# Kernel tuning notes

Measured on AMD Instinct MI355X. Metric: run time of the kernel, lower is better.

## Reference

```python
import jax, jax.numpy as jnp
import numpy as np

SP, WD, H, HID = 8, 3, 8, 256
D = HID // H
TEMP = 0.1


def setup_inputs() -> dict:
    key = jax.random.key(0)
    ks = jax.random.split(key, 14)
    B, Lq, Lk, F = 4, 1024, 2048, SP + WD
    s = 0.05
    return {
        "q_fp": jax.random.normal(ks[0], (B, Lq, F), jnp.float32),
        "v_ret": jax.random.normal(ks[1], (B, Lk, F), jnp.float32),
        "pi_star": jax.random.uniform(ks[2], (B, Lq, Lk), jnp.float32),
        "Wq_s": jax.random.normal(ks[3], (HID, SP), jnp.float32) * s,
        "bq_s": jax.random.normal(ks[4], (HID,), jnp.float32) * s,
        "Wk_s": jax.random.normal(ks[5], (HID, SP), jnp.float32) * s,
        "bk_s": jax.random.normal(ks[6], (HID,), jnp.float32) * s,
        "Wq_w": jax.random.normal(ks[7], (HID, WD), jnp.float32) * s,
        "bq_w": jax.random.normal(ks[8], (HID,), jnp.float32) * s,
        "Wk_w": jax.random.normal(ks[9], (HID, WD), jnp.float32) * s,
        "bk_w": jax.random.normal(ks[10], (HID,), jnp.float32) * s,
        "Wv": jax.random.normal(ks[11], (HID, F), jnp.float32) * s,
        "bv": jnp.zeros((HID,), jnp.float32),
        "Wo": jax.random.normal(ks[12], (HID, HID), jnp.float32) * s,
        "bo": jnp.zeros((HID,), jnp.float32),
        "wave_blend": jnp.array(0.5, jnp.float32),
    }


def _proj(x, W, b):
    # x: [B, L, F_in] -> [B, H, L, D]
    B, L, _ = x.shape
    return (x @ W.T + b).reshape(B, L, H, D).transpose(0, 2, 1, 3)


def reference(q_fp, v_ret, pi_star, Wq_s, bq_s, Wk_s, bk_s, Wq_w, bq_w, Wk_w, bk_w, Wv, bv, Wo, bo, wave_blend):
    B, Lq, _ = q_fp.shape
    # split streams: first SP dims spatial, next WD dims wave (F == SP+WD)
    q_sp, q_wv = q_fp[..., :SP], q_fp[..., SP:SP + WD]
    k_sp, k_wv = v_ret[..., :SP], v_ret[..., SP:SP + WD]
    # structural branch: scaled dot product
    q_struct = _proj(q_sp, Wq_s, bq_s)
    k_struct = _proj(k_sp, Wk_s, bk_s)
    spatial_logits = jnp.einsum('bhqd,bhkd->bhqk', q_struct, k_struct) / np.float32(np.sqrt(D))
    # wave branch: negative squared euclidean distance via norm expansion
    q_wp = _proj(q_wv, Wq_w, bq_w)
    k_wp = _proj(k_wv, Wk_w, bk_w)
    qn = jnp.sum(q_wp * q_wp, axis=-1)[..., :, None]   # [B,H,Lq,1]
    kn = jnp.sum(k_wp * k_wp, axis=-1)[..., None, :]   # [B,H,1,Lk]
    qk = jnp.einsum('bhqd,bhkd->bhqk', q_wp, k_wp)
    wave_logits = -(qn + kn - 2.0 * qk) / np.float32(TEMP)
    alpha = jax.nn.sigmoid(wave_blend)
    transport_mask = jnp.log(jnp.clip(pi_star, 1e-9, None))[:, None]  # [B,1,Lq,Lk]
    attn = jax.nn.softmax((1.0 - alpha) * spatial_logits + alpha * wave_logits + transport_mask, axis=-1)
    values = _proj(v_ret, Wv, bv)  # [B,H,Lk,D]
    ctx = jnp.einsum('bhqk,bhkd->bhqd', attn, values)
    ctx = ctx.transpose(0, 2, 1, 3).reshape(B, Lq, HID)
    return ctx @ Wo.T + bo
```

## Files before the change

### kernel.cpp

```cpp
#include <hip/hip_runtime.h>
#include <hip/hip_bf16.h>
#include <cstdint>

#define B_    4
#define LQ    1024
#define LK    2048
#define FEAT  11
#define SP_   8
#define WD_   3
#define H_    8
#define HID_  256
#define LOG2E 1.4426950408889634f
#define SPLIT 2
#define KPS   (LK / SPLIT)
#define ITERS (KPS / 64)

typedef __attribute__((ext_vector_type(4))) float f32x4;
typedef __attribute__((ext_vector_type(8))) short bf16x8;
typedef __attribute__((ext_vector_type(4))) short s16x4;

__device__ __forceinline__ float sigmoidf_(float x) { return 1.f / (1.f + __expf(-x)); }

__device__ __forceinline__ short f2bf(float f) {
  unsigned u = __float_as_uint(f);
  u += 0x7fffu + ((u >> 16) & 1u);
  return (short)(u >> 16);
}
__device__ __forceinline__ float bf2f(short s) {
  return __uint_as_float(((unsigned)(unsigned short)s) << 16);
}

__device__ __forceinline__ void gl_lds16(const void* g, void* l) {
  __builtin_amdgcn_global_load_lds(
      (const __attribute__((address_space(1))) unsigned int*)g,
      (__attribute__((address_space(3))) unsigned int*)l, 16, 0, 0);
}

__global__ __launch_bounds__(256) void proj_q_kernel(
    const float* __restrict__ q_fp, const float* __restrict__ Wq_s,
    const float* __restrict__ bq_s, const float* __restrict__ Wq_w,
    const float* __restrict__ bq_w, const float* __restrict__ wb,
    short* __restrict__ Qh)
{
  const int row = blockIdx.x;
  const int t   = threadIdx.x;
  const float alpha = sigmoidf_(wb[0]);
  const float c1 = (1.f - alpha) * 0.17677669529663687f * LOG2E;
  const float c2 = 2.f * alpha * 10.f * LOG2E;

  const float* x = q_fp + (size_t)row * FEAT;
  float xs[FEAT];
  #pragma unroll
  for (int f = 0; f < FEAT; ++f) xs[f] = x[f];

  float s = bq_s[t];
  #pragma unroll
  for (int f = 0; f < SP_; ++f) s += xs[f] * Wq_s[t * SP_ + f];
  float w = bq_w[t];
  #pragma unroll
  for (int f = 0; f < WD_; ++f) w += xs[SP_ + f] * Wq_w[t * WD_ + f];

  const int h = t >> 5, d = t & 31;
  const int b = row >> 10, q = row & (LQ - 1);
  const size_t base = ((size_t)(b * H_ + h) * LQ + q) * 64;
  Qh[base + d]      = f2bf(c1 * s);
  Qh[base + 32 + d] = f2bf(c2 * w);
}

__global__ __launch_bounds__(256) void projk_pack_kernel(
    const float* __restrict__ v_ret, const float* __restrict__ Wk_s,
    const float* __restrict__ bk_s, const float* __restrict__ Wk_w,
    const float* __restrict__ bk_w, const float* __restrict__ Wv,
    const float* __restrict__ bv,   const float* __restrict__ wb,
    short* __restrict__ KV, float* __restrict__ kb)
{
  __shared__ float ldsv[64][33];
  const int blk = blockIdx.x, bh = blockIdx.y;
  const int b = bh >> 3, h = bh & 7;
  const int t = threadIdx.x;
  const int kl = t >> 2, part = t & 3;
  const int k = blk * 64 + kl;
  const float alpha = sigmoidf_(wb[0]);

  const float* x = v_ret + (size_t)(b * LK + k) * FEAT;
  float xs[FEAT];
  #pragma unroll
  for (int f = 0; f < FEAT; ++f) xs[f] = x[f];

  float s8[8], w8[8], v8[8];
  #pragma unroll
  for (int i = 0; i < 8; ++i) {
    const int d = h * 32 + part * 8 + i;
    float s = bk_s[d];
    #pragma unroll
    for (int f = 0; f < SP_; ++f) s += xs[f] * Wk_s[d * SP_ + f];
    float w = bk_w[d];
    #pragma unroll
    for (int f = 0; f < WD_; ++f) w += xs[SP_ + f] * Wk_w[d * WD_ + f];
    float v = bv[d];
    #pragma unroll
    for (int f = 0; f < FEAT; ++f) v += xs[f] * Wv[d * FEAT + f];
    s8[i] = s; w8[i] = w; v8[i] = v;
    ldsv[kl][part * 8 + i] = v;
  }

  float sq = 0.f;
  #pragma unroll
  for (int i = 0; i < 8; ++i) sq += w8[i] * w8[i];
  sq += __shfl_xor(sq, 1);
  sq += __shfl_xor(sq, 2);
  if (part == 0) kb[(size_t)bh * LK + k] = -10.f * alpha * LOG2E * sq;

  const int a  = kl >> 5;
  const int bb = (kl >> 2) & 1;
  const int p  = kl - a * 32 - bb * 4;
  const int lo = ((p >> 3) << 2) | (p & 3);
  const int t4 = a * 2 + bb;
  const size_t base = ((size_t)bh * 32 + blk) * 768;

  bf16x8 hs, hw;
  #pragma unroll
  for (int i = 0; i < 8; ++i) { hs[i] = f2bf(s8[i]); hw[i] = f2bf(w8[i]); }
  *(bf16x8*)(KV + (base + (t4 * 2 + 0) * 64 + part * 16 + lo) * 8) = hs;
  *(bf16x8*)(KV + (base + (t4 * 2 + 1) * 64 + part * 16 + lo) * 8) = hw;

  __syncthreads();

  {
    const int j = t >> 6, l = t & 63;
    const int dt = j >> 1, kw = j & 1;
    const int lo2 = l & 15, quad = l >> 4;
    const int d = dt * 16 + lo2;
    bf16x8 hv;
    #pragma unroll
    for (int i = 0; i < 8; ++i)
      hv[i] = f2bf(ldsv[kw * 32 + quad * 8 + i][d]);
    *(bf16x8*)(KV + (base + 512 + t) * 8) = hv;
  }
}

__global__ __launch_bounds__(256) void pi_prepack_kernel(
    const float* __restrict__ pi, float* __restrict__ piP)
{
  const int Gid = blockIdx.x * 256 + threadIdx.x;
  const int g    = Gid & 255;
  const int kblk = (Gid >> 8) & 31;
  const int qt   = (Gid >> 13) & 63;
  const int b    = Gid >> 19;
  const int t4 = g >> 6, l = g & 63;
  const int lo = l & 15, quad = l >> 4;
  const int q = qt * 16 + lo;
  const int k = kblk * 64 + ((t4 >> 1) << 5) + ((t4 & 1) << 2) + quad * 8;
  const f32x4 v = *(const f32x4*)(pi + ((size_t)(b * LQ + q) * LK + k));
  *(f32x4*)(piP + (size_t)Gid * 4) = v;
}

union PF { int i[4]; bf16x8 v; };

__device__ __forceinline__ void attn_step(
    const short* __restrict__ cbuf, bf16x8 qh0, bf16x8 qh1,
    const f32x4* __restrict__ pi4, const f32x4* __restrict__ kb4,
    int lane, float& m, float& l, f32x4& o0, f32x4& o1)
{
  f32x4 st[4];
  #pragma unroll
  for (int t4 = 0; t4 < 4; ++t4) {
    const bf16x8 ka0 = *(const bf16x8*)(cbuf + ((t4 * 2 + 0) * 64 + lane) * 8);
    const bf16x8 ka1 = *(const bf16x8*)(cbuf + ((t4 * 2 + 1) * 64 + lane) * 8);
    f32x4 z = {0.f, 0.f, 0.f, 0.f};
    z = __builtin_amdgcn_mfma_f32_16x16x32_bf16(ka0, qh0, z, 0, 0, 0);
    z = __builtin_amdgcn_mfma_f32_16x16x32_bf16(ka1, qh1, z, 0, 0, 0);
    st[t4] = z;
  }

  float lg[16];
  #pragma unroll
  for (int t4 = 0; t4 < 4; ++t4) {
    #pragma unroll
    for (int r = 0; r < 4; ++r) lg[t4 * 4 + r] = st[t4][r] + kb4[t4][r];
  }

  float cm = lg[0];
  #pragma unroll
  for (int j = 1; j < 16; ++j) cm = fmaxf(cm, lg[j]);
  cm = fmaxf(cm, __shfl_xor(cm, 16));
  cm = fmaxf(cm, __shfl_xor(cm, 32));
  const float mn = fmaxf(m, cm);
  const float sc = __builtin_amdgcn_exp2f(m - mn);

  unsigned eu[16];
  #pragma unroll
  for (int t4 = 0; t4 < 4; ++t4) {
    #pragma unroll
    for (int r = 0; r < 4; ++r)
      eu[t4 * 4 + r] = __float_as_uint(
          __builtin_amdgcn_exp2f(lg[t4 * 4 + r] - mn) * pi4[t4][r]);
  }

  PF pf0, pf1;
  float ps = 0.f;
  #pragma unroll
  for (int p = 0; p < 4; ++p) {
    const int w0 = __builtin_amdgcn_perm(eu[2 * p + 1], eu[2 * p], 0x07060302u);
    const int w1 = __builtin_amdgcn_perm(eu[8 + 2 * p + 1], eu[8 + 2 * p], 0x07060302u);
    pf0.i[p] = w0; pf1.i[p] = w1;
    ps += __uint_as_float(((unsigned)w0) << 16) + __uint_as_float(w0 & 0xffff0000u);
    ps += __uint_as_float(((unsigned)w1) << 16) + __uint_as_float(w1 & 0xffff0000u);
  }
  ps += __shfl_xor(ps, 16);
  ps += __shfl_xor(ps, 32);
  l = l * sc + ps;
  m = mn;
  #pragma unroll
  for (int r = 0; r < 4; ++r) { o0[r] *= sc; o1[r] *= sc; }

  const bf16x8 va00 = *(const bf16x8*)(cbuf + ((512 + 0 * 64) + lane) * 8);
  const bf16x8 va01 = *(const bf16x8*)(cbuf + ((512 + 1 * 64) + lane) * 8);
  const bf16x8 va10 = *(const bf16x8*)(cbuf + ((512 + 2 * 64) + lane) * 8);
  const bf16x8 va11 = *(const bf16x8*)(cbuf + ((512 + 3 * 64) + lane) * 8);
  o0 = __builtin_amdgcn_mfma_f32_16x16x32_bf16(va00, pf0.v, o0, 0, 0, 0);
  o0 = __builtin_amdgcn_mfma_f32_16x16x32_bf16(va01, pf1.v, o0, 0, 0, 0);
  o1 = __builtin_amdgcn_mfma_f32_16x16x32_bf16(va10, pf0.v, o1, 0, 0, 0);
  o1 = __builtin_amdgcn_mfma_f32_16x16x32_bf16(va11, pf1.v, o1, 0, 0, 0);
}

__global__ __launch_bounds__(256, 4) void attn_kernel(
    const short* __restrict__ Qh, const short* __restrict__ KV,
    const float* __restrict__ kb, const float* __restrict__ piP,
    float* __restrict__ part)
{
  __shared__ short skv[2][6144];
  const int id = blockIdx.x;
  const int combo = id & 63;
  const int qblk  = id >> 6;
  const int bh = combo >> 1;
  const int sp = combo & 1;
  const int b = bh >> 3;
  const int wv = threadIdx.x >> 6;
  const int lane = threadIdx.x & 63;
  const int lo16 = lane & 15;
  const int quad = lane >> 4;
  const int q  = qblk * 64 + wv * 16 + lo16;
  const int qt = qblk * 4 + wv;
  const int blk0 = sp * 16;

  const size_t qoff = ((size_t)bh * LQ + q) * 64 + quad * 8;
  const bf16x8 qh0 = *(const bf16x8*)(Qh + qoff);
  const bf16x8 qh1 = *(const bf16x8*)(Qh + qoff + 32);

  const float* pibase = piP + (((size_t)(b * 64 + qt) * 32 + blk0) << 10) + lane * 4;
  const float* kbbase = kb + (size_t)bh * LK + sp * KPS + quad * 8;

  float m = -1e30f, l = 0.f;
  f32x4 o0 = {0.f, 0.f, 0.f, 0.f}, o1 = {0.f, 0.f, 0.f, 0.f};

  {
    const size_t gb = ((size_t)bh * 32 + blk0) * 768;
    #pragma unroll
    for (int c = 0; c < 3; ++c)
      gl_lds16(KV + (gb + c * 256 + wv * 64 + lane) * 8,
               &skv[0][c * 2048 + wv * 512]);
  }

  f32x4 piA[4], kbA[4], piB[4], kbB[4];
#define PI_LOAD(PID, KBD, IT) do {                                   \
    const float* pp_ = pibase + ((size_t)(IT) << 10);                \
    PID[0] = *(const f32x4*)(pp_);                                   \
    PID[1] = *(const f32x4*)(pp_ + 256);                             \
    PID[2] = *(const f32x4*)(pp_ + 512);                             \
    PID[3] = *(const f32x4*)(pp_ + 768);                             \
    const float* bp_ = kbbase + (IT) * 64;                           \
    KBD[0] = *(const f32x4*)(bp_);                                   \
    KBD[1] = *(const f32x4*)(bp_ + 4);                               \
    KBD[2] = *(const f32x4*)(bp_ + 32);                              \
    KBD[3] = *(const f32x4*)(bp_ + 36);                              \
  } while (0)

  PI_LOAD(piA, kbA, 0);

  for (int it = 0; it < ITERS; it += 2) {
    __syncthreads();
    {
      const size_t gb = ((size_t)bh * 32 + blk0 + it + 1) * 768;
      #pragma unroll
      for (int c = 0; c < 3; ++c)
        gl_lds16(KV + (gb + c * 256 + wv * 64 + lane) * 8,
                 &skv[1][c * 2048 + wv * 512]);
    }
    PI_LOAD(piB, kbB, it + 1);
    attn_step(skv[0], qh0, qh1, piA, kbA, lane, m, l, o0, o1);

    __syncthreads();
    if (it + 2 < ITERS) {
      const size_t gb = ((size_t)bh * 32 + blk0 + it + 2) * 768;
      #pragma unroll
      for (int c = 0; c < 3; ++c)
        gl_lds16(KV + (gb + c * 256 + wv * 64 + lane) * 8,
                 &skv[0][c * 2048 + wv * 512]);
      PI_LOAD(piA, kbA, it + 2);
    }
    attn_step(skv[1], qh0, qh1, piB, kbB, lane, m, l, o0, o1);
  }
#undef PI_LOAD

  float* ppart = part + ((size_t)(sp * 32 + bh) * LQ + q) * 36;
  if (quad == 0) { ppart[0] = m; ppart[1] = l; }
  *(f32x4*)(ppart + 4 + quad * 4)  = o0;
  *(f32x4*)(ppart + 20 + quad * 4) = o1;
}

__global__ __launch_bounds__(256) void wo_prep_kernel(
    const float* __restrict__ Wo, short* __restrict__ WoH, short* __restrict__ WoL)
{
  const int i = (blockIdx.x * 256 + threadIdx.x) * 4;
  const f32x4 v = *(const f32x4*)(Wo + i);
  s16x4 h, l;
  #pragma unroll
  for (int j = 0; j < 4; ++j) {
    h[j] = f2bf(v[j]);
    l[j] = f2bf(v[j] - bf2f(h[j]));
  }
  *(s16x4*)(WoH + i) = h;
  *(s16x4*)(WoL + i) = l;
}

__global__ __launch_bounds__(256) void out_kernel(
    const float* __restrict__ part, const short* __restrict__ WoH,
    const short* __restrict__ WoL, const float* __restrict__ bo,
    float* __restrict__ out)
{
  const int t = threadIdx.x;
  const int wv = t >> 6, lane = t & 63;
  const int lo16 = lane & 15, quad = lane >> 4;
  const int mt = blockIdx.x;
  const size_t gq = (size_t)mt * 16 + lo16;
  const int b = (int)(gq >> 10), qq = (int)(gq & (LQ - 1));

  bf16x8 Ah[8], Al[8];
  #pragma unroll
  for (int win = 0; win < 8; ++win) {
    const size_t r = (size_t)(b * H_ + win) * LQ + qq;
    const float* p0 = part + r * 36;
    const float* p1 = part + (r + (size_t)B_ * H_ * LQ) * 36;
    const float m0 = p0[0], l0 = p0[1], m1 = p1[0], l1 = p1[1];
    const float mM = fmaxf(m0, m1);
    const float w0 = __builtin_amdgcn_exp2f(m0 - mM);
    const float w1 = __builtin_amdgcn_exp2f(m1 - mM);
    const float inv = 1.f / (w0 * l0 + w1 * l1);
    const f32x4 a0  = *(const f32x4*)(p0 + 4 + quad * 8);
    const f32x4 a0b = *(const f32x4*)(p0 + 8 + quad * 8);
    const f32x4 a1  = *(const f32x4*)(p1 + 4 + quad * 8);
    const f32x4 a1b = *(const f32x4*)(p1 + 8 + quad * 8);
    float c8[8];
    #pragma unroll
    for (int j = 0; j < 4; ++j) {
      c8[j]     = (w0 * a0[j]  + w1 * a1[j])  * inv;
      c8[4 + j] = (w0 * a0b[j] + w1 * a1b[j]) * inv;
    }
    #pragma unroll
    for (int j = 0; j < 8; ++j) {
      const short hi = f2bf(c8[j]);
      Ah[win][j] = hi;
      Al[win][j] = f2bf(c8[j] - bf2f(hi));
    }
  }

  const int n0 = wv * 64;
  #pragma unroll
  for (int nt = 0; nt < 4; ++nt) {
    const int nb = n0 + nt * 16;
    const short* bh = WoH + (size_t)(nb + lo16) * HID_ + quad * 8;
    const short* bl = WoL + (size_t)(nb + lo16) * HID_ + quad * 8;
    const float bias = bo[nb + lo16];
    f32x4 acc = {bias, bias, bias, bias};
    #pragma unroll
    for (int win = 0; win < 8; ++win) {
      const bf16x8 Bh = *(const bf16x8*)(bh + win * 32);
      const bf16x8 Bl = *(const bf16x8*)(bl + win * 32);
      acc = __builtin_amdgcn_mfma_f32_16x16x32_bf16(Ah[win], Bh, acc, 0, 0, 0);
      acc = __builtin_amdgcn_mfma_f32_16x16x32_bf16(Al[win], Bh, acc, 0, 0, 0);
      acc = __builtin_amdgcn_mfma_f32_16x16x32_bf16(Ah[win], Bl, acc, 0, 0, 0);
    }
    #pragma unroll
    for (int r4 = 0; r4 < 4; ++r4)
      out[(size_t)(mt * 16 + quad * 4 + r4) * HID_ + nb + lo16] = acc[r4];
  }
}

extern "C" void kernel_launch(void* const* d_in, const int* in_sizes, int n_in,
                              void* d_out, int out_size, void* d_ws, size_t ws_size,
                              hipStream_t stream)
{
  const float* q_fp  = (const float*)d_in[0];
  const float* v_ret = (const float*)d_in[1];
  const float* pi    = (const float*)d_in[2];
  const float* Wq_s  = (const float*)d_in[3];
  const float* bq_s  = (const float*)d_in[4];
  const float* Wk_s  = (const float*)d_in[5];
  const float* bk_s  = (const float*)d_in[6];
  const float* Wq_w  = (const float*)d_in[7];
  const float* bq_w  = (const float*)d_in[8];
  const float* Wk_w  = (const float*)d_in[9];
  const float* bk_w  = (const float*)d_in[10];
  const float* Wv    = (const float*)d_in[11];
  const float* bv    = (const float*)d_in[12];
  const float* Wo    = (const float*)d_in[13];
  const float* bo    = (const float*)d_in[14];
  const float* wb    = (const float*)d_in[15];
  float* out = (float*)d_out;

  short* Qh   = (short*)d_ws;
  short* KV   = Qh + (size_t)2097152;
  float* kbuf = (float*)(KV + (size_t)6291456);
  float* piP  = kbuf + (size_t)65536;
  float* part = piP + (size_t)8388608;
  short* WoH  = (short*)piP;
  short* WoL  = WoH + (size_t)65536;

  proj_q_kernel<<<B_ * LQ, 256, 0, stream>>>(q_fp, Wq_s, bq_s, Wq_w, bq_w, wb, Qh);
  projk_pack_kernel<<<dim3(LK / 64, 32), 256, 0, stream>>>(
      v_ret, Wk_s, bk_s, Wk_w, bk_w, Wv, bv, wb, KV, kbuf);
  pi_prepack_kernel<<<8192, 256, 0, stream>>>(pi, piP);
  attn_kernel<<<(LQ / 64) * 32 * SPLIT, 256, 0, stream>>>(Qh, KV, kbuf, piP, part);
  wo_prep_kernel<<<64, 256, 0, stream>>>(Wo, WoH, WoL);
  out_kernel<<<(B_ * LQ) / 16, 256, 0, stream>>>(part, WoH, WoL, bo, out);
}
```

Before: 177.5 us.

## Process two query tiles per wave, split keys four ways, compute row sums via MFMA

Each wave now handles two 16-query tiles, so every K/V tile staged in shared memory feeds twice as many queries. The key range is split four ways instead of two to keep the grid size unchanged. The softmax denominator is now accumulated with an extra MFMA against a ones vector instead of per-lane bf16 unpacking plus cross-lane shuffles. The explicit register prefetch of pi and kb one step ahead is removed in favour of loads inside the step. This raises register pressure, and the output kernel now has to merge four partials per row.

```diff
diff --git a/kernel.cpp b/kernel.cpp
--- a/kernel.cpp
+++ b/kernel.cpp
@@ -11,7 +11,7 @@
 #define H_    8
 #define HID_  256
 #define LOG2E 1.4426950408889634f
-#define SPLIT 2
+#define SPLIT 4
 #define KPS   (LK / SPLIT)
 #define ITERS (KPS / 64)
 
@@ -157,71 +157,87 @@
 
 union PF { int i[4]; bf16x8 v; };
 
-__device__ __forceinline__ void attn_step(
-    const short* __restrict__ cbuf, bf16x8 qh0, bf16x8 qh1,
-    const f32x4* __restrict__ pi4, const f32x4* __restrict__ kb4,
-    int lane, float& m, float& l, f32x4& o0, f32x4& o1)
-{
-  f32x4 st[4];
+__device__ __forceinline__ void attn_step2(
+    const short* __restrict__ cbuf, const bf16x8 qh[2][2],
+    const float* __restrict__ pib0, const float* __restrict__ pib1,
+    const float* __restrict__ kbp, const bf16x8 ones, int lane,
+    float m[2], f32x4 o[2][2], f32x4 ol[2])
+{
+  f32x4 pi4[2][4];
+  #pragma unroll
+  for (int t4 = 0; t4 < 4; ++t4) {
+    pi4[0][t4] = *(const f32x4*)(pib0 + t4 * 256);
+    pi4[1][t4] = *(const f32x4*)(pib1 + t4 * 256);
+  }
+  f32x4 kb4[4];
+  kb4[0] = *(const f32x4*)(kbp);
+  kb4[1] = *(const f32x4*)(kbp + 4);
+  kb4[2] = *(const f32x4*)(kbp + 32);
+  kb4[3] = *(const f32x4*)(kbp + 36);
+
+  f32x4 st[2][4];
   #pragma unroll
   for (int t4 = 0; t4 < 4; ++t4) {
     const bf16x8 ka0 = *(const bf16x8*)(cbuf + ((t4 * 2 + 0) * 64 + lane) * 8);
     const bf16x8 ka1 = *(const bf16x8*)(cbuf + ((t4 * 2 + 1) * 64 + lane) * 8);
-    f32x4 z = {0.f, 0.f, 0.f, 0.f};
-    z = __builtin_amdgcn_mfma_f32_16x16x32_bf16(ka0, qh0, z, 0, 0, 0);
-    z = __builtin_amdgcn_mfma_f32_16x16x32_bf16(ka1, qh1, z, 0, 0, 0);
-    st[t4] = z;
-  }
-
-  float lg[16];
-  #pragma unroll
-  for (int t4 = 0; t4 < 4; ++t4) {
-    #pragma unroll
-    for (int r = 0; r < 4; ++r) lg[t4 * 4 + r] = st[t4][r] + kb4[t4][r];
-  }
-
-  float cm = lg[0];
-  #pragma unroll
-  for (int j = 1; j < 16; ++j) cm = fmaxf(cm, lg[j]);
-  cm = fmaxf(cm, __shfl_xor(cm, 16));
-  cm = fmaxf(cm, __shfl_xor(cm, 32));
-  const float mn = fmaxf(m, cm);
-  const float sc = __builtin_amdgcn_exp2f(m - mn);
-
-  unsigned eu[16];
-  #pragma unroll
-  for (int t4 = 0; t4 < 4; ++t4) {
-    #pragma unroll
-    for (int r = 0; r < 4; ++r)
-      eu[t4 * 4 + r] = __float_as_uint(
-          __builtin_amdgcn_exp2f(lg[t4 * 4 + r] - mn) * pi4[t4][r]);
-  }
-
-  PF pf0, pf1;
-  float ps = 0.f;
-  #pragma unroll
-  for (int p = 0; p < 4; ++p) {
-    const int w0 = __builtin_amdgcn_perm(eu[2 * p + 1], eu[2 * p], 0x07060302u);
-    const int w1 = __builtin_amdgcn_perm(eu[8 + 2 * p + 1], eu[8 + 2 * p], 0x07060302u);
-    pf0.i[p] = w0; pf1.i[p] = w1;
-    ps += __uint_as_float(((unsigned)w0) << 16) + __uint_as_float(w0 & 0xffff0000u);
-    ps += __uint_as_float(((unsigned)w1) << 16) + __uint_as_float(w1 & 0xffff0000u);
-  }
-  ps += __shfl_xor(ps, 16);
-  ps += __shfl_xor(ps, 32);
-  l = l * sc + ps;
-  m = mn;
-  #pragma unroll
-  for (int r = 0; r < 4; ++r) { o0[r] *= sc; o1[r] *= sc; }
+    #pragma unroll
+    for (int tl = 0; tl < 2; ++tl) {
+      f32x4 z = {0.f, 0.f, 0.f, 0.f};
+      z = __builtin_amdgcn_mfma_f32_16x16x32_bf16(ka0, qh[tl][0], z, 0, 0, 0);
+      z = __builtin_amdgcn_mfma_f32_16x16x32_bf16(ka1, qh[tl][1], z, 0, 0, 0);
+      st[tl][t4] = z;
+    }
+  }
 
   const bf16x8 va00 = *(const bf16x8*)(cbuf + ((512 + 0 * 64) + lane) * 8);
   const bf16x8 va01 = *(const bf16x8*)(cbuf + ((512 + 1 * 64) + lane) * 8);
   const bf16x8 va10 = *(const bf16x8*)(cbuf + ((512 + 2 * 64) + lane) * 8);
   const bf16x8 va11 = *(const bf16x8*)(cbuf + ((512 + 3 * 64) + lane) * 8);
-  o0 = __builtin_amdgcn_mfma_f32_16x16x32_bf16(va00, pf0.v, o0, 0, 0, 0);
-  o0 = __builtin_amdgcn_mfma_f32_16x16x32_bf16(va01, pf1.v, o0, 0, 0, 0);
-  o1 = __builtin_amdgcn_mfma_f32_16x16x32_bf16(va10, pf0.v, o1, 0, 0, 0);
-  o1 = __builtin_amdgcn_mfma_f32_16x16x32_bf16(va11, pf1.v, o1, 0, 0, 0);
+
+  #pragma unroll
+  for (int tl = 0; tl < 2; ++tl) {
+    float lg[16];
+    #pragma unroll
+    for (int t4 = 0; t4 < 4; ++t4) {
+      #pragma unroll
+      for (int r = 0; r < 4; ++r) lg[t4 * 4 + r] = st[tl][t4][r] + kb4[t4][r];
+    }
+
+    float cm = lg[0];
+    #pragma unroll
+    for (int j = 1; j < 16; ++j) cm = fmaxf(cm, lg[j]);
+    cm = fmaxf(cm, __shfl_xor(cm, 16));
+    cm = fmaxf(cm, __shfl_xor(cm, 32));
+    const float mn = fmaxf(m[tl], cm);
+    const float sc = __builtin_amdgcn_exp2f(m[tl] - mn);
+    m[tl] = mn;
+
+    unsigned eu[16];
+    #pragma unroll
+    for (int t4 = 0; t4 < 4; ++t4) {
+      #pragma unroll
+      for (int r = 0; r < 4; ++r)
+        eu[t4 * 4 + r] = __float_as_uint(
+            __builtin_amdgcn_exp2f(lg[t4 * 4 + r] - mn) * pi4[tl][t4][r]);
+    }
+
+    PF pf0, pf1;
+    #pragma unroll
+    for (int p = 0; p < 4; ++p) {
+      pf0.i[p] = __builtin_amdgcn_perm(eu[2 * p + 1], eu[2 * p], 0x07060302u);
+      pf1.i[p] = __builtin_amdgcn_perm(eu[8 + 2 * p + 1], eu[8 + 2 * p], 0x07060302u);
+    }
+
+    #pragma unroll
+    for (int r = 0; r < 4; ++r) { o[tl][0][r] *= sc; o[tl][1][r] *= sc; ol[tl][r] *= sc; }
+
+    o[tl][0] = __builtin_amdgcn_mfma_f32_16x16x32_bf16(va00, pf0.v, o[tl][0], 0, 0, 0);
+    o[tl][0] = __builtin_amdgcn_mfma_f32_16x16x32_bf16(va01, pf1.v, o[tl][0], 0, 0, 0);
+    o[tl][1] = __builtin_amdgcn_mfma_f32_16x16x32_bf16(va10, pf0.v, o[tl][1], 0, 0, 0);
+    o[tl][1] = __builtin_amdgcn_mfma_f32_16x16x32_bf16(va11, pf1.v, o[tl][1], 0, 0, 0);
+    ol[tl] = __builtin_amdgcn_mfma_f32_16x16x32_bf16(ones, pf0.v, ol[tl], 0, 0, 0);
+    ol[tl] = __builtin_amdgcn_mfma_f32_16x16x32_bf16(ones, pf1.v, ol[tl], 0, 0, 0);
+  }
 }
 
 __global__ __launch_bounds__(256, 4) void attn_kernel(
@@ -231,28 +247,38 @@
 {
   __shared__ short skv[2][6144];
   const int id = blockIdx.x;
-  const int combo = id & 63;
-  const int qblk  = id >> 6;
-  const int bh = combo >> 1;
-  const int sp = combo & 1;
+  const int combo = id & 127;
+  const int qblk  = id >> 7;
+  const int bh = combo >> 2;
+  const int sp = combo & 3;
   const int b = bh >> 3;
   const int wv = threadIdx.x >> 6;
   const int lane = threadIdx.x & 63;
   const int lo16 = lane & 15;
   const int quad = lane >> 4;
-  const int q  = qblk * 64 + wv * 16 + lo16;
-  const int qt = qblk * 4 + wv;
-  const int blk0 = sp * 16;
-
-  const size_t qoff = ((size_t)bh * LQ + q) * 64 + quad * 8;
-  const bf16x8 qh0 = *(const bf16x8*)(Qh + qoff);
-  const bf16x8 qh1 = *(const bf16x8*)(Qh + qoff + 32);
-
-  const float* pibase = piP + (((size_t)(b * 64 + qt) * 32 + blk0) << 10) + lane * 4;
+  const int qt0 = qblk * 8 + wv * 2;
+  const int blk0 = sp * ITERS;
+
+  bf16x8 qh[2][2];
+  #pragma unroll
+  for (int tl = 0; tl < 2; ++tl) {
+    const size_t qoff = ((size_t)bh * LQ + (qt0 + tl) * 16 + lo16) * 64 + quad * 8;
+    qh[tl][0] = *(const bf16x8*)(Qh + qoff);
+    qh[tl][1] = *(const bf16x8*)(Qh + qoff + 32);
+  }
+
+  const float* pib0 = piP + (((size_t)(b * 64 + qt0) * 32 + blk0) << 10) + lane * 4;
+  const float* pib1 = piP + (((size_t)(b * 64 + qt0 + 1) * 32 + blk0) << 10) + lane * 4;
   const float* kbbase = kb + (size_t)bh * LK + sp * KPS + quad * 8;
 
-  float m = -1e30f, l = 0.f;
-  f32x4 o0 = {0.f, 0.f, 0.f, 0.f}, o1 = {0.f, 0.f, 0.f, 0.f};
+  bf16x8 ones;
+  #pragma unroll
+  for (int j = 0; j < 8; ++j) ones[j] = (lo16 == 0) ? (short)0x3F80 : (short)0;
+
+  float m[2] = {-1e30f, -1e30f};
+  f32x4 o[2][2] = {{{0.f,0.f,0.f,0.f},{0.f,0.f,0.f,0.f}},
+                   {{0.f,0.f,0.f,0.f},{0.f,0.f,0.f,0.f}}};
+  f32x4 ol[2] = {{0.f,0.f,0.f,0.f},{0.f,0.f,0.f,0.f}};
 
   {
     const size_t gb = ((size_t)bh * 32 + blk0) * 768;
@@ -261,22 +287,6 @@
       gl_lds16(KV + (gb + c * 256 + wv * 64 + lane) * 8,
                &skv[0][c * 2048 + wv * 512]);
   }
-
-  f32x4 piA[4], kbA[4], piB[4], kbB[4];
-#define PI_LOAD(PID, KBD, IT) do {                                   \
-    const float* pp_ = pibase + ((size_t)(IT) << 10);                \
-    PID[0] = *(const f32x4*)(pp_);                                   \
-    PID[1] = *(const f32x4*)(pp_ + 256);                             \
-    PID[2] = *(const f32x4*)(pp_ + 512);                             \
-    PID[3] = *(const f32x4*)(pp_ + 768);                             \
-    const float* bp_ = kbbase + (IT) * 64;                           \
-    KBD[0] = *(const f32x4*)(bp_);                                   \
-    KBD[1] = *(const f32x4*)(bp_ + 4);                               \
-    KBD[2] = *(const f32x4*)(bp_ + 32);                              \
-    KBD[3] = *(const f32x4*)(bp_ + 36);                              \
-  } while (0)
-
-  PI_LOAD(piA, kbA, 0);
 
   for (int it = 0; it < ITERS; it += 2) {
     __syncthreads();
@@ -287,8 +297,8 @@
         gl_lds16(KV + (gb + c * 256 + wv * 64 + lane) * 8,
                  &skv[1][c * 2048 + wv * 512]);
     }
-    PI_LOAD(piB, kbB, it + 1);
-    attn_step(skv[0], qh0, qh1, piA, kbA, lane, m, l, o0, o1);
+    attn_step2(skv[0], qh, pib0 + ((size_t)it << 10), pib1 + ((size_t)it << 10),
+               kbbase + it * 64, ones, lane, m, o, ol);
 
     __syncthreads();
     if (it + 2 < ITERS) {
@@ -297,16 +307,19 @@
       for (int c = 0; c < 3; ++c)
         gl_lds16(KV + (gb + c * 256 + wv * 64 + lane) * 8,
                  &skv[0][c * 2048 + wv * 512]);
-      PI_LOAD(piA, kbA, it + 2);
-    }
-    attn_step(skv[1], qh0, qh1, piB, kbB, lane, m, l, o0, o1);
-  }
-#undef PI_LOAD
-
-  float* ppart = part + ((size_t)(sp * 32 + bh) * LQ + q) * 36;
-  if (quad == 0) { ppart[0] = m; ppart[1] = l; }
-  *(f32x4*)(ppart + 4 + quad * 4)  = o0;
-  *(f32x4*)(ppart + 20 + quad * 4) = o1;
+    }
+    attn_step2(skv[1], qh, pib0 + ((size_t)(it + 1) << 10), pib1 + ((size_t)(it + 1) << 10),
+               kbbase + (it + 1) * 64, ones, lane, m, o, ol);
+  }
+
+  #pragma unroll
+  for (int tl = 0; tl < 2; ++tl) {
+    const int q = (qt0 + tl) * 16 + lo16;
+    float* ppart = part + ((size_t)(sp * 32 + bh) * LQ + q) * 36;
+    if (quad == 0) { ppart[0] = m[tl]; ppart[1] = ol[tl][0]; }
+    *(f32x4*)(ppart + 4 + quad * 4)  = o[tl][0];
+    *(f32x4*)(ppart + 20 + quad * 4) = o[tl][1];
+  }
 }
 
 __global__ __launch_bounds__(256) void wo_prep_kernel(
@@ -340,28 +353,43 @@
   #pragma unroll
   for (int win = 0; win < 8; ++win) {
     const size_t r = (size_t)(b * H_ + win) * LQ + qq;
-    const float* p0 = part + r * 36;
-    const float* p1 = part + (r + (size_t)B_ * H_ * LQ) * 36;
-    const float m0 = p0[0], l0 = p0[1], m1 = p1[0], l1 = p1[1];
-    const float mM = fmaxf(m0, m1);
-    const float w0 = __builtin_amdgcn_exp2f(m0 - mM);
-    const float w1 = __builtin_amdgcn_exp2f(m1 - mM);
-    const float inv = 1.f / (w0 * l0 + w1 * l1);
-    const f32x4 a0  = *(const f32x4*)(p0 + 4 + quad * 8);
-    const f32x4 a0b = *(const f32x4*)(p0 + 8 + quad * 8);
-    const f32x4 a1  = *(const f32x4*)(p1 + 4 + quad * 8);
-    const f32x4 a1b = *(const f32x4*)(p1 + 8 + quad * 8);
+    const float* p[SPLIT];
+    float ms[SPLIT], ls[SPLIT];
+    #pragma unroll
+    for (int s = 0; s < SPLIT; ++s) {
+      p[s] = part + (r + (size_t)s * (B_ * H_ * LQ)) * 36;
+      ms[s] = p[s][0]; ls[s] = p[s][1];
+    }
+    float mM = ms[0];
+    #pragma unroll
+    for (int s = 1; s < SPLIT; ++s) mM = fmaxf(mM, ms[s]);
+    float ws[SPLIT], den = 0.f;
+    #pragma unroll
+    for (int s = 0; s < SPLIT; ++s) {
+      ws[s] = __builtin_amdgcn_exp2f(ms[s] - mM);
+      den += ws[s] * ls[s];
+    }
+    const float inv = 1.f / den;
+
     float c8[8];
     #pragma unroll
-    for (int j = 0; j < 4; ++j) {
-      c8[j]     = (w0 * a0[j]  + w1 * a1[j])  * inv;
-      c8[4 + j] = (w0 * a0b[j] + w1 * a1b[j]) * inv;
+    for (int j = 0; j < 8; ++j) c8[j] = 0.f;
+    #pragma unroll
+    for (int s = 0; s < SPLIT; ++s) {
+      const f32x4 a0 = *(const f32x4*)(p[s] + 4 + quad * 8);
+      const f32x4 a1 = *(const f32x4*)(p[s] + 8 + quad * 8);
+      #pragma unroll
+      for (int j = 0; j < 4; ++j) {
+        c8[j]     += ws[s] * a0[j];
+        c8[4 + j] += ws[s] * a1[j];
+      }
     }
     #pragma unroll
     for (int j = 0; j < 8; ++j) {
-      const short hi = f2bf(c8[j]);
+      const float cv = c8[j] * inv;
+      const short hi = f2bf(cv);
       Ah[win][j] = hi;
-      Al[win][j] = f2bf(c8[j] - bf2f(hi));
+      Al[win][j] = f2bf(cv - bf2f(hi));
     }
   }
 
@@ -421,7 +449,7 @@
   projk_pack_kernel<<<dim3(LK / 64, 32), 256, 0, stream>>>(
       v_ret, Wk_s, bk_s, Wk_w, bk_w, Wv, bv, wb, KV, kbuf);
   pi_prepack_kernel<<<8192, 256, 0, stream>>>(pi, piP);
-  attn_kernel<<<(LQ / 64) * 32 * SPLIT, 256, 0, stream>>>(Qh, KV, kbuf, piP, part);
+  attn_kernel<<<(LQ / 128) * 32 * SPLIT, 256, 0, stream>>>(Qh, KV, kbuf, piP, part);
   wo_prep_kernel<<<64, 256, 0, stream>>>(Wo, WoH, WoL);
   out_kernel<<<(B_ * LQ) / 16, 256, 0, stream>>>(part, WoH, WoL, bo, out);
 }
```

Result: slower. 181.6 us (+2.3%).
